# Kernel optimization log

Measured on AMD Instinct MI355X. Metric: run time of the kernel, lower is better.

Reference implementation:

```python
import jax, jax.numpy as jnp
import numpy as np
import math

B, S, D, H = 2, 2048, 1024, 16


def setup_inputs() -> dict:
    key = jax.random.key(0)
    ks = jax.random.split(key, 5)
    sc = 0.02  # small init scale for weights
    return {
        "x": jax.random.normal(ks[0], (B, S, D), dtype=jnp.float32),
        "Wqkv_w": jax.random.normal(ks[1], (3 * D, D), dtype=jnp.float32) * sc,
        "Wqkv_b": jnp.zeros((3 * D,), jnp.float32),
        "sel_w": jax.random.normal(ks[2], (1, D), dtype=jnp.float32) * sc,
        "sel_b": jnp.zeros((1,), jnp.float32),
        "out_w": jax.random.normal(ks[3], (D, D), dtype=jnp.float32) * sc,
        "out_b": jnp.zeros((D,), jnp.float32),
    }


def reference(x, Wqkv_w, Wqkv_b, sel_w, sel_b, out_w, out_b):
    b, s, d = x.shape
    h = H
    hd = d // h
    # Wqkv projection -> (b, s, 3, h, hd)
    qkv = (x @ Wqkv_w.T + Wqkv_b).reshape(b, s, 3, h, hd)
    q, k, v = qkv[:, :, 0], qkv[:, :, 1], qkv[:, :, 2]
    scale = 1.0 / math.sqrt(hd)
    scores = jnp.einsum('bthd,bshd->bhts', q, k * scale)  # (b,h,s,s)
    causal_mask = jnp.triu(jnp.full((s, s), -10000.0, dtype=scores.dtype), 1)
    attn = jax.nn.softmax(scores + causal_mask, axis=-1)
    ctx = jnp.einsum('bhts,bshd->bthd', attn, v).reshape(b, s, d)
    attn_out = ctx @ out_w.T + out_b  # (b,s,d)
    # selection: softmax over sequence dim, scaled by sqrt(d)/8
    sel = jax.nn.softmax(x @ sel_w.T + sel_b, axis=1) * (math.sqrt(d) / 8.0)  # (b,s,1)
    # eval path: topk over sequence, gather, scatter_add into x
    kk = math.ceil(math.sqrt(s))  # 46 for s=2048
    _, idx = jax.lax.top_k(sel[..., 0], kk)  # (b,kk) indices into seq dim
    val = attn_out * sel  # (b,s,d)
    bidx = jnp.arange(b)[:, None]
    src = val[bidx, idx]  # gather -> (b,kk,d)
    y = x.at[bidx, idx].add(src)  # scatter_add
    return y
```

## Files before the change

### kernel.cpp

```cpp
#include <hip/hip_runtime.h>
#include <stdint.h>

#define BATCH 2
#define SEQ   2048
#define DIM   1024
#define NH    16
#define HD    64
#define KK    46
#define NSEL  (BATCH*KK)
#define MPAD  128
#define CHUNK 128
#define NCH   (SEQ/CHUNK)
#define QP    48
#define SPLITK 8

typedef __attribute__((ext_vector_type(8))) short short8;
typedef __attribute__((ext_vector_type(4))) float f32x4;

__device__ inline unsigned short f2bf(float f) {
  union { float f; uint32_t u; } v; v.f = f;
  uint32_t u = v.u;
  uint32_t r = u + 0x7fff + ((u >> 16) & 1);
  return (unsigned short)(r >> 16);
}
__device__ inline float bf2f(unsigned short h) {
  union { uint32_t u; float f; } v; v.u = ((uint32_t)h) << 16;
  return v.f;
}
__device__ inline uint32_t f2ord(float f) {
  union { float f; uint32_t u; } v; v.f = f;
  return (v.u & 0x80000000u) ? ~v.u : (v.u | 0x80000000u);
}

__device__ inline void gload16(const void* g, void* l) {
  __builtin_amdgcn_global_load_lds(
      (const __attribute__((address_space(1))) void*)g,
      (__attribute__((address_space(3))) void*)l, 16, 0, 0);
}

__global__ __launch_bounds__(256) void prep_kernel(
    const float* __restrict__ wqkv, const float* __restrict__ outw,
    unsigned short* __restrict__ wqkvb, unsigned short* __restrict__ outwb,
    const float* __restrict__ x, unsigned short* __restrict__ xb,
    const float* __restrict__ sel_w, const float* __restrict__ sel_b,
    float* __restrict__ z, float* __restrict__ out)
{
  if (blockIdx.x < 2048) {
    int i = (blockIdx.x * 256 + threadIdx.x) * 8;
    const int NW = 3 * DIM * DIM;
    const float* src; unsigned short* dst; int j;
    if (i < NW) { src = wqkv; dst = wqkvb; j = i; }
    else        { src = outw; dst = outwb; j = i - NW; }
    float4 a = *(const float4*)(src + j);
    float4 b = *(const float4*)(src + j + 4);
    ushort4 o0, o1;
    o0.x = f2bf(a.x); o0.y = f2bf(a.y); o0.z = f2bf(a.z); o0.w = f2bf(a.w);
    o1.x = f2bf(b.x); o1.y = f2bf(b.y); o1.z = f2bf(b.z); o1.w = f2bf(b.w);
    *(ushort4*)(dst + j)     = o0;
    *(ushort4*)(dst + j + 4) = o1;
  } else {
    int wave = threadIdx.x >> 6, lane = threadIdx.x & 63;
    int row = (blockIdx.x - 2048) * 4 + wave;
    const float* xr = x + (size_t)row * DIM;
    unsigned short* xo = xb + (size_t)row * DIM;
    float* oo = out + (size_t)row * DIM;
    float s = 0.f;
#pragma unroll
    for (int it = 0; it < 4; ++it) {
      int c = it * 256 + lane * 4;
      float4 xv = *(const float4*)(xr + c);
      float4 wv = *(const float4*)(sel_w + c);
      s += xv.x*wv.x + xv.y*wv.y + xv.z*wv.z + xv.w*wv.w;
      ushort4 o;
      o.x = f2bf(xv.x); o.y = f2bf(xv.y); o.z = f2bf(xv.z); o.w = f2bf(xv.w);
      *(ushort4*)(xo + c) = o;
      *(float4*)(oo + c) = xv;
    }
#pragma unroll
    for (int o = 32; o > 0; o >>= 1) s += __shfl_xor(s, o);
    if (lane == 0) z[row] = s + sel_b[0];
  }
}

__global__ __launch_bounds__(256) void topk_kernel(const float* __restrict__ z,
                                                   float* __restrict__ sel,
                                                   int* __restrict__ idxout)
{
  int b = blockIdx.x, t = threadIdx.x;
  int lane = t & 63, wid = t >> 6;
  __shared__ int   hist[256];
  __shared__ float fred[4];
  __shared__ int   ired[4];
  __shared__ int   s_B, s_need;
  __shared__ float s_mx, s_sum;

  int s0 = t * 8;
  float zz[8];
  uint32_t uu[8];
  {
    float4 a = *(const float4*)(z + b*SEQ + s0);
    float4 c = *(const float4*)(z + b*SEQ + s0 + 4);
    zz[0]=a.x; zz[1]=a.y; zz[2]=a.z; zz[3]=a.w;
    zz[4]=c.x; zz[5]=c.y; zz[6]=c.z; zz[7]=c.w;
  }
#pragma unroll
  for (int i = 0; i < 8; ++i) uu[i] = f2ord(zz[i]);

  float lm = zz[0];
#pragma unroll
  for (int i = 1; i < 8; ++i) lm = fmaxf(lm, zz[i]);
#pragma unroll
  for (int o = 32; o > 0; o >>= 1) lm = fmaxf(lm, __shfl_xor(lm, o));
  if (lane == 0) fred[wid] = lm;
  __syncthreads();
  if (t == 0) s_mx = fmaxf(fmaxf(fred[0], fred[1]), fmaxf(fred[2], fred[3]));
  __syncthreads();
  float mx = s_mx;

  float pp[8];
  float ls = 0.f;
#pragma unroll
  for (int i = 0; i < 8; ++i) { pp[i] = __expf(zz[i] - mx); ls += pp[i]; }
#pragma unroll
  for (int o = 32; o > 0; o >>= 1) ls += __shfl_xor(ls, o);
  if (lane == 0) fred[wid] = ls;
  __syncthreads();
  if (t == 0) s_sum = fred[0] + fred[1] + fred[2] + fred[3];
  __syncthreads();
  float sscale = 4.0f / s_sum;
#pragma unroll
  for (int i = 0; i < 8; ++i) sel[b*SEQ + s0 + i] = pp[i] * sscale;

  uint32_t pref = 0;
  int need = KK;
#pragma unroll
  for (int pass = 0; pass < 4; ++pass) {
    int shift = 24 - pass * 8;
    uint32_t maskhi = pass ? (0xFFFFFFFFu << (shift + 8)) : 0u;
    hist[t] = 0;
    __syncthreads();
#pragma unroll
    for (int i = 0; i < 8; ++i) {
      if ((uu[i] & maskhi) == pref)
        atomicAdd(&hist[(uu[i] >> shift) & 255], 1);
    }
    __syncthreads();
    if (t < 64) {
      int c0 = hist[t*4], c1 = hist[t*4+1], c2 = hist[t*4+2], c3 = hist[t*4+3];
      int sl = c0 + c1 + c2 + c3;
      int suf = sl;
#pragma unroll
      for (int off = 1; off < 64; off <<= 1) {
        int o = __shfl_down(suf, off);
        if (lane + off < 64) suf += o;
      }
      int above = suf - sl;
      if (above < need && above + sl >= need) {
        int cum = above;
        int cs[4] = {c0, c1, c2, c3};
#pragma unroll
        for (int k = 3; k >= 0; --k) {
          if (cum < need && cum + cs[k] >= need) {
            s_B = t*4 + k;
            s_need = need - cum;
            break;
          }
          cum += cs[k];
        }
      }
    }
    __syncthreads();
    pref |= ((uint32_t)s_B) << shift;
    need = s_need;
    __syncthreads();
  }
  uint32_t T = pref;

  int cgt = 0, ceq = 0;
#pragma unroll
  for (int i = 0; i < 8; ++i) { cgt += (uu[i] > T); ceq += (uu[i] == T); }
  int pack = (cgt << 12) | ceq;
  int inc = pack;
#pragma unroll
  for (int off = 1; off < 64; off <<= 1) {
    int o = __shfl_up(inc, off);
    if (lane >= off) inc += o;
  }
  if (lane == 63) ired[wid] = inc;
  __syncthreads();
  int wbase = 0;
  if (wid == 1) wbase = ired[0];
  else if (wid == 2) wbase = ired[0] + ired[1];
  else if (wid == 3) wbase = ired[0] + ired[1] + ired[2];
  int ex = wbase + inc - pack;
  int g = ex >> 12, e = ex & 0xFFF;
#pragma unroll
  for (int i = 0; i < 8; ++i) {
    int s = s0 + i;
    bool isgt = uu[i] > T;
    bool iseq = uu[i] == T;
    int rank = -1;
    if (isgt) rank = g + (e < need ? e : need);
    else if (iseq && e < need) rank = g + e;
    if (rank >= 0) idxout[b*KK + rank] = s;
    g += isgt; e += iseq;
  }
}

__global__ __launch_bounds__(256) void gemms_kernel(
    const unsigned short* __restrict__ xb,
    const unsigned short* __restrict__ wqkvb,
    const float* __restrict__ Wqkv_b,
    unsigned short* __restrict__ kvb,
    float* __restrict__ qpart,
    const int* __restrict__ idxp)
{
  __shared__ unsigned short As[2][128*32];
  __shared__ unsigned short Bs[2][128*32];
  int tid  = threadIdx.x;
  int lane = tid & 63, wave = tid >> 6;
  int wr = (wave >> 1) * 64, wc = (wave & 1) * 64;
  int lr = lane & 15;
  int sx = (((lane >> 4) ^ ((lane >> 1) & 3)) << 3);
  int srow = lane >> 2;
  int scol = (((lane & 3) ^ ((lane >> 3) & 3)) << 3);
  int rb = 4 * (lane >> 4);

  if (blockIdx.x < 512) {
    const unsigned short* Bw = wqkvb + (size_t)DIM * DIM;
    int flat = blockIdx.x;
    int xcd = flat & 7, i8 = flat >> 3;
    int tile = xcd * 64 + i8;
    int bx = tile & 15, by = tile >> 4;
    int bm = by * 128, bn = bx * 128;
    const int K = DIM, N = 2 * DIM;

    const unsigned short* ap[2];
    const unsigned short* bp[2];
#pragma unroll
    for (int c = 0; c < 2; ++c) {
      int row = (wave * 2 + c) * 16 + srow;
      ap[c] = xb + (size_t)(bm + row) * K + scol;
      bp[c] = Bw + (size_t)(bn + row) * K + scol;
    }
    f32x4 acc[4][4] = {};
#pragma unroll
    for (int c = 0; c < 2; ++c) {
      int ch = wave * 2 + c;
      gload16(ap[c], (char*)As[0] + ch * 1024 + lane * 16);
      gload16(bp[c], (char*)Bs[0] + ch * 1024 + lane * 16);
      ap[c] += 32; bp[c] += 32;
    }
    __syncthreads();
    int cur = 0;
    for (int t = 0; t < 32; ++t) {
      if (t + 1 < 32) {
#pragma unroll
        for (int c = 0; c < 2; ++c) {
          int ch = wave * 2 + c;
          gload16(ap[c], (char*)As[cur ^ 1] + ch * 1024 + lane * 16);
          gload16(bp[c], (char*)Bs[cur ^ 1] + ch * 1024 + lane * 16);
          ap[c] += 32; bp[c] += 32;
        }
      }
      short8 af[4], bf[4];
#pragma unroll
      for (int m = 0; m < 4; ++m) af[m] = *(const short8*)&As[cur][(wr + m*16 + lr)*32 + sx];
#pragma unroll
      for (int n = 0; n < 4; ++n) bf[n] = *(const short8*)&Bs[cur][(wc + n*16 + lr)*32 + sx];
#pragma unroll
      for (int m = 0; m < 4; ++m)
#pragma unroll
        for (int n = 0; n < 4; ++n)
          acc[m][n] = __builtin_amdgcn_mfma_f32_16x16x32_bf16(af[m], bf[n], acc[m][n], 0, 0, 0);
      __syncthreads();
      cur ^= 1;
    }
#pragma unroll
    for (int m = 0; m < 4; ++m) {
#pragma unroll
      for (int n = 0; n < 4; ++n) {
        int col = bn + wc + n*16 + lr;
        float bv = Wqkv_b[DIM + col];
#pragma unroll
        for (int i = 0; i < 4; ++i) {
          int row = bm + wr + m*16 + rb + i;
          kvb[(size_t)row * N + col] = f2bf(acc[m][n][i] + bv);
        }
      }
    }
  } else {
    int bi = blockIdx.x - 512;
    int sk = bi >> 3;
    int bn = (bi & 7) * 128;
    int kb = sk * 128;
    const int K = DIM, N = DIM;

    const unsigned short* ap[2];
    const unsigned short* bp[2];
#pragma unroll
    for (int c = 0; c < 2; ++c) {
      int row = (wave * 2 + c) * 16 + srow;
      int bb = 0, rr = 0;
      if (row < NSEL) { bb = row / KK; rr = idxp[row]; }
      ap[c] = xb + ((size_t)(bb * SEQ + rr)) * K + kb + scol;
      bp[c] = wqkvb + (size_t)(bn + row) * K + kb + scol;
    }
    f32x4 acc[4][4] = {};
#pragma unroll
    for (int c = 0; c < 2; ++c) {
      int ch = wave * 2 + c;
      gload16(ap[c], (char*)As[0] + ch * 1024 + lane * 16);
      gload16(bp[c], (char*)Bs[0] + ch * 1024 + lane * 16);
      ap[c] += 32; bp[c] += 32;
    }
    __syncthreads();
    int cur = 0;
    for (int t = 0; t < 4; ++t) {
      if (t + 1 < 4) {
#pragma unroll
        for (int c = 0; c < 2; ++c) {
          int ch = wave * 2 + c;
          gload16(ap[c], (char*)As[cur ^ 1] + ch * 1024 + lane * 16);
          gload16(bp[c], (char*)Bs[cur ^ 1] + ch * 1024 + lane * 16);
          ap[c] += 32; bp[c] += 32;
        }
      }
      short8 af[4], bf[4];
#pragma unroll
      for (int m = 0; m < 4; ++m) af[m] = *(const short8*)&As[cur][(wr + m*16 + lr)*32 + sx];
#pragma unroll
      for (int n = 0; n < 4; ++n) bf[n] = *(const short8*)&Bs[cur][(wc + n*16 + lr)*32 + sx];
#pragma unroll
      for (int m = 0; m < 4; ++m)
#pragma unroll
        for (int n = 0; n < 4; ++n)
          acc[m][n] = __builtin_amdgcn_mfma_f32_16x16x32_bf16(af[m], bf[n], acc[m][n], 0, 0, 0);
      __syncthreads();
      cur ^= 1;
    }
    float* po = qpart + (size_t)sk * MPAD * N;
#pragma unroll
    for (int m = 0; m < 4; ++m) {
#pragma unroll
      for (int n = 0; n < 4; ++n) {
        int col = bn + wc + n*16 + lr;
#pragma unroll
        for (int i = 0; i < 4; ++i) {
          int row = wr + m*16 + rb + i;
          po[(size_t)row * N + col] = acc[m][n][i];
        }
      }
    }
  }
}

__global__ __launch_bounds__(256) void gemm_splitk_kernel(
    const unsigned short* __restrict__ A,
    const unsigned short* __restrict__ Bw,
    float* __restrict__ part, int N, int K)
{
  __shared__ unsigned short As[2][128*32];
  __shared__ unsigned short Bs[2][128*32];
  int tid  = threadIdx.x;
  int lane = tid & 63, wave = tid >> 6;
  int wr = (wave >> 1) * 64, wc = (wave & 1) * 64;
  int bn = blockIdx.x * 128;
  int sk = blockIdx.z;
  int ksl = K / SPLITK;
  int kb  = sk * ksl;

  int lr = lane & 15;
  int sx = (((lane >> 4) ^ ((lane >> 1) & 3)) << 3);
  int srow = lane >> 2;
  int scol = (((lane & 3) ^ ((lane >> 3) & 3)) << 3);

  const unsigned short* ap[2];
  const unsigned short* bp[2];
#pragma unroll
  for (int c = 0; c < 2; ++c) {
    int row = (wave * 2 + c) * 16 + srow;
    ap[c] = A  + (size_t)row * K + kb + scol;
    bp[c] = Bw + (size_t)(bn + row) * K + kb + scol;
  }

  f32x4 acc[4][4] = {};
  int nt = ksl / 32;
#pragma unroll
  for (int c = 0; c < 2; ++c) {
    int ch = wave * 2 + c;
    gload16(ap[c], (char*)As[0] + ch * 1024 + lane * 16);
    gload16(bp[c], (char*)Bs[0] + ch * 1024 + lane * 16);
    ap[c] += 32; bp[c] += 32;
  }
  __syncthreads();

  int cur = 0;
  for (int t = 0; t < nt; ++t) {
    if (t + 1 < nt) {
#pragma unroll
      for (int c = 0; c < 2; ++c) {
        int ch = wave * 2 + c;
        gload16(ap[c], (char*)As[cur ^ 1] + ch * 1024 + lane * 16);
        gload16(bp[c], (char*)Bs[cur ^ 1] + ch * 1024 + lane * 16);
        ap[c] += 32; bp[c] += 32;
      }
    }
    short8 af[4], bf[4];
#pragma unroll
    for (int m = 0; m < 4; ++m) af[m] = *(const short8*)&As[cur][(wr + m*16 + lr)*32 + sx];
#pragma unroll
    for (int n = 0; n < 4; ++n) bf[n] = *(const short8*)&Bs[cur][(wc + n*16 + lr)*32 + sx];
#pragma unroll
    for (int m = 0; m < 4; ++m)
#pragma unroll
      for (int n = 0; n < 4; ++n)
        acc[m][n] = __builtin_amdgcn_mfma_f32_16x16x32_bf16(af[m], bf[n], acc[m][n], 0, 0, 0);
    __syncthreads();
    cur ^= 1;
  }

  int rb = 4 * (lane >> 4);
  float* po = part + (size_t)sk * MPAD * N;
#pragma unroll
  for (int m = 0; m < 4; ++m) {
#pragma unroll
    for (int n = 0; n < 4; ++n) {
      int col = bn + wc + n*16 + lr;
#pragma unroll
      for (int i = 0; i < 4; ++i) {
        int row = wr + m*16 + rb + i;
        po[(size_t)row * N + col] = acc[m][n][i];
      }
    }
  }
}

__global__ void qcombine_kernel(const float* __restrict__ part,
                                const float* __restrict__ bias,
                                unsigned short* __restrict__ qgb)
{
  int i = (blockIdx.x * 256 + threadIdx.x) * 4;
  int col = i & (DIM - 1);
  float4 a = *(const float4*)(bias + col);
#pragma unroll
  for (int sk = 0; sk < SPLITK; ++sk) {
    float4 p = *(const float4*)(part + (size_t)sk * MPAD * DIM + i);
    a.x += p.x; a.y += p.y; a.z += p.z; a.w += p.w;
  }
  ushort4 o;
  o.x = f2bf(a.x); o.y = f2bf(a.y); o.z = f2bf(a.z); o.w = f2bf(a.w);
  *(ushort4*)(qgb + i) = o;
}

__global__ __launch_bounds__(256) void attn_chunk_kernel(
    const unsigned short* __restrict__ qgb,
    const unsigned short* __restrict__ kvb,
    const int* __restrict__ idx,
    float* __restrict__ Opart,
    float* __restrict__ mpart,
    float* __restrict__ lpart)
{
  int h = blockIdx.x, b = blockIdx.y, kc = blockIdx.z;
  int t = threadIdx.x, lane = t & 63, w = t >> 6;
  int lr = lane & 15, hk = lane >> 4;

  __shared__ unsigned short Qs[QP][72];
  __shared__ union { unsigned short Ks[CHUNK][72]; unsigned short ps[QP][136]; } U;
  __shared__ unsigned short Vt[HD][134];
  __shared__ int   rsi[QP];
  __shared__ float wred[4][QP];
  __shared__ float wsum[4][QP];

  if (t < QP) rsi[t] = (t < KK) ? idx[b*KK + t] : -1;
  for (int i = t; i < QP*8; i += 256) {
    int q = i >> 3, c8 = (i & 7) * 8;
    uint4 v;
    if (q < KK) v = *(const uint4*)(qgb + (size_t)(b*KK + q)*DIM + h*HD + c8);
    else        { v.x = 0; v.y = 0; v.z = 0; v.w = 0; }
    *(uint4*)&Qs[q][c8] = v;
  }
  for (int i = t; i < CHUNK*8; i += 256) {
    int r = i >> 3, c8 = (i & 7) * 8;
    *(uint4*)&U.Ks[r][c8] =
      *(const uint4*)(kvb + ((size_t)(b*SEQ + kc*CHUNK + r))*2048 + h*HD + c8);
  }
  for (int i = t; i < CHUNK*8; i += 256) {
    int r = i >> 3, d8 = (i & 7) * 8;
    uint4 v = *(const uint4*)(kvb + ((size_t)(b*SEQ + kc*CHUNK + r))*2048 + DIM + h*HD + d8);
    const unsigned short* pv = (const unsigned short*)&v;
#pragma unroll
    for (int j = 0; j < 8; ++j) Vt[d8 + j][r] = pv[j];
  }
  __syncthreads();

  short8 af[3][2], bfr[2][2];
#pragma unroll
  for (int m = 0; m < 3; ++m)
#pragma unroll
    for (int kk = 0; kk < 2; ++kk)
      af[m][kk] = *(const short8*)&Qs[m*16 + lr][kk*32 + hk*8];
#pragma unroll
  for (int j = 0; j < 2; ++j)
#pragma unroll
    for (int kk = 0; kk < 2; ++kk)
      bfr[j][kk] = *(const short8*)&U.Ks[(2*w + j)*16 + lr][kk*32 + hk*8];
  f32x4 acc[3][2] = {};
#pragma unroll
  for (int kk = 0; kk < 2; ++kk)
#pragma unroll
    for (int m = 0; m < 3; ++m)
#pragma unroll
      for (int j = 0; j < 2; ++j)
        acc[m][j] = __builtin_amdgcn_mfma_f32_16x16x32_bf16(af[m][kk], bfr[j][kk], acc[m][j], 0, 0, 0);

  float s[3][2][4];
  float rmax[3][4];
#pragma unroll
  for (int m = 0; m < 3; ++m)
#pragma unroll
    for (int reg = 0; reg < 4; ++reg) {
      int row = m*16 + hk*4 + reg;
      int rq = rsi[row];
      float mx = -3e38f;
#pragma unroll
      for (int j = 0; j < 2; ++j) {
        int gkey = kc*CHUNK + (2*w + j)*16 + lr;
        float v = acc[m][j][reg] * 0.125f;
        if (gkey > rq) v = -3e38f;
        s[m][j][reg] = v;
        mx = fmaxf(mx, v);
      }
#pragma unroll
      for (int o = 1; o < 16; o <<= 1) mx = fmaxf(mx, __shfl_xor(mx, o));
      rmax[m][reg] = mx;
    }
  if (lr == 0) {
#pragma unroll
    for (int m = 0; m < 3; ++m)
#pragma unroll
      for (int reg = 0; reg < 4; ++reg)
        wred[w][m*16 + hk*4 + reg] = rmax[m][reg];
  }
  __syncthreads();

  float rsum[3][4];
#pragma unroll
  for (int m = 0; m < 3; ++m)
#pragma unroll
    for (int reg = 0; reg < 4; ++reg) {
      int row = m*16 + hk*4 + reg;
      float gm = fmaxf(fmaxf(wred[0][row], wred[1][row]), fmaxf(wred[2][row], wred[3][row]));
      gm = fmaxf(gm, -1e37f);
      float sum = 0.f;
#pragma unroll
      for (int j = 0; j < 2; ++j) {
        float p = __expf(s[m][j][reg] - gm);
        sum += p;
        U.ps[row][(2*w + j)*16 + lr] = f2bf(p);
      }
#pragma unroll
      for (int o = 1; o < 16; o <<= 1) sum += __shfl_xor(sum, o);
      rsum[m][reg] = sum;
      rmax[m][reg] = gm;
    }
  if (lr == 0) {
#pragma unroll
    for (int m = 0; m < 3; ++m)
#pragma unroll
      for (int reg = 0; reg < 4; ++reg)
        wsum[w][m*16 + hk*4 + reg] = rsum[m][reg];
  }
  __syncthreads();

  if (w == 0 && lr == 0) {
    size_t base = ((size_t)(b*NH + h)*NCH + kc)*KK;
#pragma unroll
    for (int m = 0; m < 3; ++m)
#pragma unroll
      for (int reg = 0; reg < 4; ++reg) {
        int row = m*16 + hk*4 + reg;
        if (row < KK) {
          float L = wsum[0][row] + wsum[1][row] + wsum[2][row] + wsum[3][row];
          mpart[base + row] = rmax[m][reg];
          lpart[base + row] = L;
        }
      }
  }

  f32x4 acc2[3] = {};
#pragma unroll
  for (int kt = 0; kt < 4; ++kt) {
    short8 bv = *(const short8*)&Vt[w*16 + lr][kt*32 + hk*8];
#pragma unroll
    for (int m = 0; m < 3; ++m) {
      short8 av = *(const short8*)&U.ps[m*16 + lr][kt*32 + hk*8];
      acc2[m] = __builtin_amdgcn_mfma_f32_16x16x32_bf16(av, bv, acc2[m], 0, 0, 0);
    }
  }
  size_t obase = (((size_t)(b*NH + h)*NCH + kc)*KK)*HD;
#pragma unroll
  for (int m = 0; m < 3; ++m)
#pragma unroll
    for (int reg = 0; reg < 4; ++reg) {
      int q = m*16 + hk*4 + reg;
      if (q < KK) Opart[obase + (size_t)q*HD + w*16 + lr] = acc2[m][reg];
    }
}

__global__ __launch_bounds__(64) void attn_combine_kernel(
    const float* __restrict__ Opart,
    const float* __restrict__ mpart,
    const float* __restrict__ lpart,
    unsigned short* __restrict__ ctxg)
{
  int h = blockIdx.x, j = blockIdx.y;
  int b = j / KK, q = j % KK;
  int d = threadIdx.x;
  size_t mb = (size_t)(b*NH + h)*NCH;
  float M = -3e38f;
#pragma unroll
  for (int c = 0; c < NCH; ++c) M = fmaxf(M, mpart[(mb + c)*KK + q]);
  float L = 0.f, o = 0.f;
#pragma unroll
  for (int c = 0; c < NCH; ++c) {
    float f = __expf(mpart[(mb + c)*KK + q] - M);
    L += lpart[(mb + c)*KK + q] * f;
    o = fmaf(Opart[((mb + c)*KK + q)*HD + d], f, o);
  }
  ctxg[(size_t)j*DIM + h*HD + d] = f2bf(o / L);
}

__global__ void rowfix_kernel(const float* __restrict__ x,
                              const float* __restrict__ apart,
                              const float* __restrict__ out_b,
                              const float* __restrict__ sel,
                              const int* __restrict__ idx,
                              float* __restrict__ out)
{
  int j = blockIdx.x;
  int b = j / KK;
  int r = idx[j];
  int col = threadIdx.x * 4;
  size_t off = ((size_t)(b * SEQ + r)) * DIM + col;
  float s = sel[b * SEQ + r];
  float4 a = *(const float4*)(out_b + col);
#pragma unroll
  for (int sk = 0; sk < SPLITK; ++sk) {
    float4 p = *(const float4*)(apart + ((size_t)sk * MPAD + j) * DIM + col);
    a.x += p.x; a.y += p.y; a.z += p.z; a.w += p.w;
  }
  float4 v = *(const float4*)(x + off);
  v.x += a.x * s; v.y += a.y * s; v.z += a.z * s; v.w += a.w * s;
  *(float4*)(out + off) = v;
}

extern "C" void kernel_launch(void* const* d_in, const int* in_sizes, int n_in,
                              void* d_out, int out_size, void* d_ws, size_t ws_size,
                              hipStream_t stream)
{
  (void)in_sizes; (void)n_in; (void)out_size; (void)ws_size;
  const float* x      = (const float*)d_in[0];
  const float* Wqkv_w = (const float*)d_in[1];
  const float* Wqkv_b = (const float*)d_in[2];
  const float* sel_w  = (const float*)d_in[3];
  const float* sel_b  = (const float*)d_in[4];
  const float* out_w  = (const float*)d_in[5];
  const float* out_b  = (const float*)d_in[6];
  float* out = (float*)d_out;
  char* ws = (char*)d_ws;

  unsigned short* xb    = (unsigned short*)(ws);
  unsigned short* wqkvb = (unsigned short*)(ws + (8u  << 20));
  unsigned short* outwb = (unsigned short*)(ws + (14u << 20));
  unsigned short* kvb   = (unsigned short*)(ws + (16u << 20));
  float* z      = (float*)(ws + (32u << 20));
  float* sel    = (float*)(ws + (32u << 20) + (16u << 10));
  int*   idx    = (int*)  (ws + (32u << 20) + (32u << 10));
  unsigned short* ctxg = (unsigned short*)(ws + (33u << 20) + (256u << 10));
  unsigned short* qgb  = (unsigned short*)(ws + (33u << 20) + (512u << 10));
  float* Opart = (float*)(ws + (35u << 20));
  float* mpart = (float*)(ws + (42u << 20));
  float* lpart = (float*)(ws + (42u << 20) + (256u << 10));
  float* qpart = (float*)(ws + (44u << 20));
  float* apart = (float*)(ws + (48u << 20));

  prep_kernel<<<3072, 256, 0, stream>>>(Wqkv_w, out_w, wqkvb, outwb,
                                        x, xb, sel_w, sel_b, z, out);
  topk_kernel<<<BATCH, 256, 0, stream>>>(z, sel, idx);

  gemms_kernel<<<576, 256, 0, stream>>>(xb, wqkvb, Wqkv_b, kvb, qpart, idx);
  qcombine_kernel<<<MPAD*DIM/1024, 256, 0, stream>>>(qpart, Wqkv_b, qgb);

  dim3 gac(NH, BATCH, NCH);
  attn_chunk_kernel<<<gac, 256, 0, stream>>>(qgb, kvb, idx, Opart, mpart, lpart);
  dim3 gcb(NH, NSEL);
  attn_combine_kernel<<<gcb, 64, 0, stream>>>(Opart, mpart, lpart, ctxg);

  dim3 gsk(DIM/128, 1, SPLITK);
  gemm_splitk_kernel<<<gsk, 256, 0, stream>>>(ctxg, outwb, apart, DIM, DIM);

  rowfix_kernel<<<NSEL, 256, 0, stream>>>(x, apart, out_b, sel, idx, out);
}
```

Baseline: 76.14 us.

## Use single-wave 64x64 GEMM tiles, drop Q split-K and its combine kernel

Both GEMM kernels now run one 64-lane wave per block on 64x64 tiles, with barrier-free double buffering that waits on vmcnt. The K/V projection becomes 2048 smaller tiles. The selected-row Q projection runs the full K loop per tile and writes bf16 output with bias directly, which removes the qpart buffer and the qcombine launch. The out-projection uses 64x64 tiles over two M blocks, so it only covers the 92 real rows plus a little padding. The trade-off is less data reuse per block and lower per-block MFMA occupancy, while the Q path loses its split-K parallelism.

```diff
diff --git a/kernel.cpp b/kernel.cpp
--- a/kernel.cpp
+++ b/kernel.cpp
@@ -207,250 +207,194 @@
   }
 }
 
-__global__ __launch_bounds__(256) void gemms_kernel(
+__global__ __launch_bounds__(64) void gemms_kernel(
     const unsigned short* __restrict__ xb,
     const unsigned short* __restrict__ wqkvb,
     const float* __restrict__ Wqkv_b,
     unsigned short* __restrict__ kvb,
-    float* __restrict__ qpart,
+    unsigned short* __restrict__ qgb,
     const int* __restrict__ idxp)
 {
-  __shared__ unsigned short As[2][128*32];
-  __shared__ unsigned short Bs[2][128*32];
-  int tid  = threadIdx.x;
-  int lane = tid & 63, wave = tid >> 6;
-  int wr = (wave >> 1) * 64, wc = (wave & 1) * 64;
+  __shared__ unsigned short As[2][64*32];
+  __shared__ unsigned short Bs[2][64*32];
+  int lane = threadIdx.x;
   int lr = lane & 15;
   int sx = (((lane >> 4) ^ ((lane >> 1) & 3)) << 3);
-  int srow = lane >> 2;
+  int crow = lane >> 2;
   int scol = (((lane & 3) ^ ((lane >> 3) & 3)) << 3);
   int rb = 4 * (lane >> 4);
 
-  if (blockIdx.x < 512) {
+  const unsigned short* ap[4];
+  const unsigned short* bp[4];
+  int bm, bn, nt;
+  bool isKV = blockIdx.x < 2048;
+  const int K = DIM;
+
+  if (isKV) {
+    int flat = blockIdx.x;
+    int tile = (flat & 7) * 256 + (flat >> 3);
+    int bx = tile & 31, by = tile >> 5;
+    bm = by * 64; bn = bx * 64;
+    nt = 32;
     const unsigned short* Bw = wqkvb + (size_t)DIM * DIM;
-    int flat = blockIdx.x;
-    int xcd = flat & 7, i8 = flat >> 3;
-    int tile = xcd * 64 + i8;
-    int bx = tile & 15, by = tile >> 4;
-    int bm = by * 128, bn = bx * 128;
-    const int K = DIM, N = 2 * DIM;
-
-    const unsigned short* ap[2];
-    const unsigned short* bp[2];
-#pragma unroll
-    for (int c = 0; c < 2; ++c) {
-      int row = (wave * 2 + c) * 16 + srow;
+#pragma unroll
+    for (int c = 0; c < 4; ++c) {
+      int row = c * 16 + crow;
       ap[c] = xb + (size_t)(bm + row) * K + scol;
       bp[c] = Bw + (size_t)(bn + row) * K + scol;
     }
-    f32x4 acc[4][4] = {};
-#pragma unroll
-    for (int c = 0; c < 2; ++c) {
-      int ch = wave * 2 + c;
-      gload16(ap[c], (char*)As[0] + ch * 1024 + lane * 16);
-      gload16(bp[c], (char*)Bs[0] + ch * 1024 + lane * 16);
-      ap[c] += 32; bp[c] += 32;
-    }
-    __syncthreads();
-    int cur = 0;
-    for (int t = 0; t < 32; ++t) {
-      if (t + 1 < 32) {
-#pragma unroll
-        for (int c = 0; c < 2; ++c) {
-          int ch = wave * 2 + c;
-          gload16(ap[c], (char*)As[cur ^ 1] + ch * 1024 + lane * 16);
-          gload16(bp[c], (char*)Bs[cur ^ 1] + ch * 1024 + lane * 16);
-          ap[c] += 32; bp[c] += 32;
-        }
-      }
-      short8 af[4], bf[4];
-#pragma unroll
-      for (int m = 0; m < 4; ++m) af[m] = *(const short8*)&As[cur][(wr + m*16 + lr)*32 + sx];
-#pragma unroll
-      for (int n = 0; n < 4; ++n) bf[n] = *(const short8*)&Bs[cur][(wc + n*16 + lr)*32 + sx];
-#pragma unroll
-      for (int m = 0; m < 4; ++m)
-#pragma unroll
-        for (int n = 0; n < 4; ++n)
-          acc[m][n] = __builtin_amdgcn_mfma_f32_16x16x32_bf16(af[m], bf[n], acc[m][n], 0, 0, 0);
-      __syncthreads();
-      cur ^= 1;
-    }
+  } else {
+    int bi = blockIdx.x - 2048;
+    bm = (bi >> 4) * 64;
+    bn = (bi & 15) * 64;
+    nt = 32;
+#pragma unroll
+    for (int c = 0; c < 4; ++c) {
+      int row = bm + c * 16 + crow;
+      int bb = 0, rr = 0;
+      if (row < NSEL) { bb = row / KK; rr = idxp[row]; }
+      ap[c] = xb + ((size_t)(bb * SEQ + rr)) * K + scol;
+      bp[c] = wqkvb + (size_t)(bn + c * 16 + crow) * K + scol;
+    }
+  }
+
+#pragma unroll
+  for (int c = 0; c < 4; ++c) {
+    gload16(ap[c], (char*)As[0] + c * 1024 + lane * 16);
+    gload16(bp[c], (char*)Bs[0] + c * 1024 + lane * 16);
+    ap[c] += 32; bp[c] += 32;
+  }
+
+  f32x4 acc[4][4] = {};
+  for (int t = 0; t < nt; ++t) {
+    asm volatile("s_waitcnt vmcnt(0)" ::: "memory");
+    __builtin_amdgcn_sched_barrier(0);
+    int cur = t & 1;
+    short8 af[4], bf[4];
+#pragma unroll
+    for (int m = 0; m < 4; ++m) af[m] = *(const short8*)&As[cur][(m*16 + lr)*32 + sx];
+#pragma unroll
+    for (int n = 0; n < 4; ++n) bf[n] = *(const short8*)&Bs[cur][(n*16 + lr)*32 + sx];
+    if (t + 1 < nt) {
+#pragma unroll
+      for (int c = 0; c < 4; ++c) {
+        gload16(ap[c], (char*)As[cur ^ 1] + c * 1024 + lane * 16);
+        gload16(bp[c], (char*)Bs[cur ^ 1] + c * 1024 + lane * 16);
+        ap[c] += 32; bp[c] += 32;
+      }
+    }
+#pragma unroll
+    for (int m = 0; m < 4; ++m)
+#pragma unroll
+      for (int n = 0; n < 4; ++n)
+        acc[m][n] = __builtin_amdgcn_mfma_f32_16x16x32_bf16(af[m], bf[n], acc[m][n], 0, 0, 0);
+  }
+
+  if (isKV) {
+    const int N = 2 * DIM;
 #pragma unroll
     for (int m = 0; m < 4; ++m) {
 #pragma unroll
       for (int n = 0; n < 4; ++n) {
-        int col = bn + wc + n*16 + lr;
+        int col = bn + n*16 + lr;
         float bv = Wqkv_b[DIM + col];
 #pragma unroll
         for (int i = 0; i < 4; ++i) {
-          int row = bm + wr + m*16 + rb + i;
+          int row = bm + m*16 + rb + i;
           kvb[(size_t)row * N + col] = f2bf(acc[m][n][i] + bv);
         }
       }
     }
   } else {
-    int bi = blockIdx.x - 512;
-    int sk = bi >> 3;
-    int bn = (bi & 7) * 128;
-    int kb = sk * 128;
-    const int K = DIM, N = DIM;
-
-    const unsigned short* ap[2];
-    const unsigned short* bp[2];
-#pragma unroll
-    for (int c = 0; c < 2; ++c) {
-      int row = (wave * 2 + c) * 16 + srow;
-      int bb = 0, rr = 0;
-      if (row < NSEL) { bb = row / KK; rr = idxp[row]; }
-      ap[c] = xb + ((size_t)(bb * SEQ + rr)) * K + kb + scol;
-      bp[c] = wqkvb + (size_t)(bn + row) * K + kb + scol;
-    }
-    f32x4 acc[4][4] = {};
-#pragma unroll
-    for (int c = 0; c < 2; ++c) {
-      int ch = wave * 2 + c;
-      gload16(ap[c], (char*)As[0] + ch * 1024 + lane * 16);
-      gload16(bp[c], (char*)Bs[0] + ch * 1024 + lane * 16);
-      ap[c] += 32; bp[c] += 32;
-    }
-    __syncthreads();
-    int cur = 0;
-    for (int t = 0; t < 4; ++t) {
-      if (t + 1 < 4) {
-#pragma unroll
-        for (int c = 0; c < 2; ++c) {
-          int ch = wave * 2 + c;
-          gload16(ap[c], (char*)As[cur ^ 1] + ch * 1024 + lane * 16);
-          gload16(bp[c], (char*)Bs[cur ^ 1] + ch * 1024 + lane * 16);
-          ap[c] += 32; bp[c] += 32;
+#pragma unroll
+    for (int m = 0; m < 4; ++m) {
+#pragma unroll
+      for (int n = 0; n < 4; ++n) {
+        int col = bn + n*16 + lr;
+        float bv = Wqkv_b[col];
+#pragma unroll
+        for (int i = 0; i < 4; ++i) {
+          int row = bm + m*16 + rb + i;
+          if (row < NSEL) qgb[(size_t)row * DIM + col] = f2bf(acc[m][n][i] + bv);
         }
       }
-      short8 af[4], bf[4];
-#pragma unroll
-      for (int m = 0; m < 4; ++m) af[m] = *(const short8*)&As[cur][(wr + m*16 + lr)*32 + sx];
-#pragma unroll
-      for (int n = 0; n < 4; ++n) bf[n] = *(const short8*)&Bs[cur][(wc + n*16 + lr)*32 + sx];
-#pragma unroll
-      for (int m = 0; m < 4; ++m)
-#pragma unroll
-        for (int n = 0; n < 4; ++n)
-          acc[m][n] = __builtin_amdgcn_mfma_f32_16x16x32_bf16(af[m], bf[n], acc[m][n], 0, 0, 0);
-      __syncthreads();
-      cur ^= 1;
-    }
-    float* po = qpart + (size_t)sk * MPAD * N;
-#pragma unroll
-    for (int m = 0; m < 4; ++m) {
-#pragma unroll
-      for (int n = 0; n < 4; ++n) {
-        int col = bn + wc + n*16 + lr;
-#pragma unroll
-        for (int i = 0; i < 4; ++i) {
-          int row = wr + m*16 + rb + i;
-          po[(size_t)row * N + col] = acc[m][n][i];
-        }
-      }
-    }
-  }
-}
-
-__global__ __launch_bounds__(256) void gemm_splitk_kernel(
+    }
+  }
+}
+
+__global__ __launch_bounds__(64) void outproj_kernel(
     const unsigned short* __restrict__ A,
     const unsigned short* __restrict__ Bw,
-    float* __restrict__ part, int N, int K)
-{
-  __shared__ unsigned short As[2][128*32];
-  __shared__ unsigned short Bs[2][128*32];
-  int tid  = threadIdx.x;
-  int lane = tid & 63, wave = tid >> 6;
-  int wr = (wave >> 1) * 64, wc = (wave & 1) * 64;
-  int bn = blockIdx.x * 128;
-  int sk = blockIdx.z;
-  int ksl = K / SPLITK;
-  int kb  = sk * ksl;
-
+    float* __restrict__ part)
+{
+  __shared__ unsigned short As[2][64*32];
+  __shared__ unsigned short Bs[2][64*32];
+  int lane = threadIdx.x;
   int lr = lane & 15;
   int sx = (((lane >> 4) ^ ((lane >> 1) & 3)) << 3);
-  int srow = lane >> 2;
+  int crow = lane >> 2;
   int scol = (((lane & 3) ^ ((lane >> 3) & 3)) << 3);
-
-  const unsigned short* ap[2];
-  const unsigned short* bp[2];
-#pragma unroll
-  for (int c = 0; c < 2; ++c) {
-    int row = (wave * 2 + c) * 16 + srow;
-    ap[c] = A  + (size_t)row * K + kb + scol;
+  int rb = 4 * (lane >> 4);
+
+  int bn = blockIdx.x * 64;
+  int bm = blockIdx.y * 64;
+  int sk = blockIdx.z;
+  int kb = sk * (DIM / SPLITK);
+  const int K = DIM, nt = (DIM / SPLITK) / 32;
+
+  const unsigned short* ap[4];
+  const unsigned short* bp[4];
+#pragma unroll
+  for (int c = 0; c < 4; ++c) {
+    int row = c * 16 + crow;
+    ap[c] = A  + (size_t)(bm + row) * K + kb + scol;
     bp[c] = Bw + (size_t)(bn + row) * K + kb + scol;
   }
+#pragma unroll
+  for (int c = 0; c < 4; ++c) {
+    gload16(ap[c], (char*)As[0] + c * 1024 + lane * 16);
+    gload16(bp[c], (char*)Bs[0] + c * 1024 + lane * 16);
+    ap[c] += 32; bp[c] += 32;
+  }
 
   f32x4 acc[4][4] = {};
-  int nt = ksl / 32;
-#pragma unroll
-  for (int c = 0; c < 2; ++c) {
-    int ch = wave * 2 + c;
-    gload16(ap[c], (char*)As[0] + ch * 1024 + lane * 16);
-    gload16(bp[c], (char*)Bs[0] + ch * 1024 + lane * 16);
-    ap[c] += 32; bp[c] += 32;
-  }
-  __syncthreads();
-
-  int cur = 0;
   for (int t = 0; t < nt; ++t) {
+    asm volatile("s_waitcnt vmcnt(0)" ::: "memory");
+    __builtin_amdgcn_sched_barrier(0);
+    int cur = t & 1;
+    short8 af[4], bf[4];
+#pragma unroll
+    for (int m = 0; m < 4; ++m) af[m] = *(const short8*)&As[cur][(m*16 + lr)*32 + sx];
+#pragma unroll
+    for (int n = 0; n < 4; ++n) bf[n] = *(const short8*)&Bs[cur][(n*16 + lr)*32 + sx];
     if (t + 1 < nt) {
 #pragma unroll
-      for (int c = 0; c < 2; ++c) {
-        int ch = wave * 2 + c;
-        gload16(ap[c], (char*)As[cur ^ 1] + ch * 1024 + lane * 16);
-        gload16(bp[c], (char*)Bs[cur ^ 1] + ch * 1024 + lane * 16);
+      for (int c = 0; c < 4; ++c) {
+        gload16(ap[c], (char*)As[cur ^ 1] + c * 1024 + lane * 16);
+        gload16(bp[c], (char*)Bs[cur ^ 1] + c * 1024 + lane * 16);
         ap[c] += 32; bp[c] += 32;
       }
     }
-    short8 af[4], bf[4];
-#pragma unroll
-    for (int m = 0; m < 4; ++m) af[m] = *(const short8*)&As[cur][(wr + m*16 + lr)*32 + sx];
-#pragma unroll
-    for (int n = 0; n < 4; ++n) bf[n] = *(const short8*)&Bs[cur][(wc + n*16 + lr)*32 + sx];
 #pragma unroll
     for (int m = 0; m < 4; ++m)
 #pragma unroll
       for (int n = 0; n < 4; ++n)
         acc[m][n] = __builtin_amdgcn_mfma_f32_16x16x32_bf16(af[m], bf[n], acc[m][n], 0, 0, 0);
-    __syncthreads();
-    cur ^= 1;
-  }
-
-  int rb = 4 * (lane >> 4);
-  float* po = part + (size_t)sk * MPAD * N;
+  }
+
+  float* po = part + (size_t)sk * MPAD * DIM;
 #pragma unroll
   for (int m = 0; m < 4; ++m) {
 #pragma unroll
     for (int n = 0; n < 4; ++n) {
-      int col = bn + wc + n*16 + lr;
+      int col = bn + n*16 + lr;
 #pragma unroll
       for (int i = 0; i < 4; ++i) {
-        int row = wr + m*16 + rb + i;
-        po[(size_t)row * N + col] = acc[m][n][i];
-      }
-    }
-  }
-}
-
-__global__ void qcombine_kernel(const float* __restrict__ part,
-                                const float* __restrict__ bias,
-                                unsigned short* __restrict__ qgb)
-{
-  int i = (blockIdx.x * 256 + threadIdx.x) * 4;
-  int col = i & (DIM - 1);
-  float4 a = *(const float4*)(bias + col);
-#pragma unroll
-  for (int sk = 0; sk < SPLITK; ++sk) {
-    float4 p = *(const float4*)(part + (size_t)sk * MPAD * DIM + i);
-    a.x += p.x; a.y += p.y; a.z += p.z; a.w += p.w;
-  }
-  ushort4 o;
-  o.x = f2bf(a.x); o.y = f2bf(a.y); o.z = f2bf(a.z); o.w = f2bf(a.w);
-  *(ushort4*)(qgb + i) = o;
+        int row = bm + m*16 + rb + i;
+        po[(size_t)row * DIM + col] = acc[m][n][i];
+      }
+    }
+  }
 }
 
 __global__ __launch_bounds__(256) void attn_chunk_kernel(
@@ -682,23 +626,21 @@
   float* Opart = (float*)(ws + (35u << 20));
   float* mpart = (float*)(ws + (42u << 20));
   float* lpart = (float*)(ws + (42u << 20) + (256u << 10));
-  float* qpart = (float*)(ws + (44u << 20));
   float* apart = (float*)(ws + (48u << 20));
 
   prep_kernel<<<3072, 256, 0, stream>>>(Wqkv_w, out_w, wqkvb, outwb,
                                         x, xb, sel_w, sel_b, z, out);
   topk_kernel<<<BATCH, 256, 0, stream>>>(z, sel, idx);
 
-  gemms_kernel<<<576, 256, 0, stream>>>(xb, wqkvb, Wqkv_b, kvb, qpart, idx);
-  qcombine_kernel<<<MPAD*DIM/1024, 256, 0, stream>>>(qpart, Wqkv_b, qgb);
+  gemms_kernel<<<2080, 64, 0, stream>>>(xb, wqkvb, Wqkv_b, kvb, qgb, idx);
 
   dim3 gac(NH, BATCH, NCH);
   attn_chunk_kernel<<<gac, 256, 0, stream>>>(qgb, kvb, idx, Opart, mpart, lpart);
   dim3 gcb(NH, NSEL);
   attn_combine_kernel<<<gcb, 64, 0, stream>>>(Opart, mpart, lpart, ctxg);
 
-  dim3 gsk(DIM/128, 1, SPLITK);
-  gemm_splitk_kernel<<<gsk, 256, 0, stream>>>(ctxg, outwb, apart, DIM, DIM);
+  dim3 gop(16, 2, SPLITK);
+  outproj_kernel<<<gop, 64, 0, stream>>>(ctxg, outwb, apart);
 
   rowfix_kernel<<<NSEL, 256, 0, stream>>>(x, apart, out_b, sel, idx, out);
 }
```

After: 83.52 us. +9.7%, slower.

## Triple-buffer GEMM LDS tiles with one barrier per K-step and vmcnt waits

Applied to the files above, without the earlier changes.

Moves the GEMM main loops from double-buffered to triple-buffered shared-memory staging. Two tiles are prefetched ahead, each step waits with explicit s_waitcnt vmcnt, and one raw s_barrier per iteration replaces the trailing __syncthreads. This aims to hide global-load latency better and halve barrier count, at the cost of 50% more LDS per block (48KB), which could reduce occupancy. The split-K kernel now hardcodes nt=4, assuming K/SPLITK==128.

```diff
diff --git a/kernel.cpp b/kernel.cpp
--- a/kernel.cpp
+++ b/kernel.cpp
@@ -215,8 +215,8 @@
     float* __restrict__ qpart,
     const int* __restrict__ idxp)
 {
-  __shared__ unsigned short As[2][128*32];
-  __shared__ unsigned short Bs[2][128*32];
+  __shared__ unsigned short As[3][128*32];
+  __shared__ unsigned short Bs[3][128*32];
   int tid  = threadIdx.x;
   int lane = tid & 63, wave = tid >> 6;
   int wr = (wave >> 1) * 64, wc = (wave & 1) * 64;
@@ -233,7 +233,7 @@
     int tile = xcd * 64 + i8;
     int bx = tile & 15, by = tile >> 4;
     int bm = by * 128, bn = bx * 128;
-    const int K = DIM, N = 2 * DIM;
+    const int K = DIM, N = 2 * DIM, nt = 32;
 
     const unsigned short* ap[2];
     const unsigned short* bp[2];
@@ -245,36 +245,43 @@
     }
     f32x4 acc[4][4] = {};
 #pragma unroll
-    for (int c = 0; c < 2; ++c) {
-      int ch = wave * 2 + c;
-      gload16(ap[c], (char*)As[0] + ch * 1024 + lane * 16);
-      gload16(bp[c], (char*)Bs[0] + ch * 1024 + lane * 16);
-      ap[c] += 32; bp[c] += 32;
-    }
-    __syncthreads();
+    for (int pb = 0; pb < 2; ++pb) {
+#pragma unroll
+      for (int c = 0; c < 2; ++c) {
+        int ch = wave * 2 + c;
+        gload16(ap[c], (char*)As[pb] + ch * 1024 + lane * 16);
+        gload16(bp[c], (char*)Bs[pb] + ch * 1024 + lane * 16);
+        ap[c] += 32; bp[c] += 32;
+      }
+    }
     int cur = 0;
-    for (int t = 0; t < 32; ++t) {
-      if (t + 1 < 32) {
+    for (int t = 0; t < nt; ++t) {
+      if (t + 1 < nt) asm volatile("s_waitcnt vmcnt(4)" ::: "memory");
+      else            asm volatile("s_waitcnt vmcnt(0)" ::: "memory");
+      __builtin_amdgcn_s_barrier();
+      asm volatile("" ::: "memory");
+      __builtin_amdgcn_sched_barrier(0);
+      short8 af[4], bf[4];
+#pragma unroll
+      for (int m = 0; m < 4; ++m) af[m] = *(const short8*)&As[cur][(wr + m*16 + lr)*32 + sx];
+#pragma unroll
+      for (int n = 0; n < 4; ++n) bf[n] = *(const short8*)&Bs[cur][(wc + n*16 + lr)*32 + sx];
+      if (t + 2 < nt) {
+        int nb = cur + 2; if (nb >= 3) nb -= 3;
 #pragma unroll
         for (int c = 0; c < 2; ++c) {
           int ch = wave * 2 + c;
-          gload16(ap[c], (char*)As[cur ^ 1] + ch * 1024 + lane * 16);
-          gload16(bp[c], (char*)Bs[cur ^ 1] + ch * 1024 + lane * 16);
+          gload16(ap[c], (char*)As[nb] + ch * 1024 + lane * 16);
+          gload16(bp[c], (char*)Bs[nb] + ch * 1024 + lane * 16);
           ap[c] += 32; bp[c] += 32;
         }
       }
-      short8 af[4], bf[4];
-#pragma unroll
-      for (int m = 0; m < 4; ++m) af[m] = *(const short8*)&As[cur][(wr + m*16 + lr)*32 + sx];
-#pragma unroll
-      for (int n = 0; n < 4; ++n) bf[n] = *(const short8*)&Bs[cur][(wc + n*16 + lr)*32 + sx];
 #pragma unroll
       for (int m = 0; m < 4; ++m)
 #pragma unroll
         for (int n = 0; n < 4; ++n)
           acc[m][n] = __builtin_amdgcn_mfma_f32_16x16x32_bf16(af[m], bf[n], acc[m][n], 0, 0, 0);
-      __syncthreads();
-      cur ^= 1;
+      cur = (cur + 1 == 3) ? 0 : cur + 1;
     }
 #pragma unroll
     for (int m = 0; m < 4; ++m) {
@@ -294,7 +301,7 @@
     int sk = bi >> 3;
     int bn = (bi & 7) * 128;
     int kb = sk * 128;
-    const int K = DIM, N = DIM;
+    const int K = DIM, N = DIM, nt = 4;
 
     const unsigned short* ap[2];
     const unsigned short* bp[2];
@@ -308,36 +315,43 @@
     }
     f32x4 acc[4][4] = {};
 #pragma unroll
-    for (int c = 0; c < 2; ++c) {
-      int ch = wave * 2 + c;
-      gload16(ap[c], (char*)As[0] + ch * 1024 + lane * 16);
-      gload16(bp[c], (char*)Bs[0] + ch * 1024 + lane * 16);
-      ap[c] += 32; bp[c] += 32;
-    }
-    __syncthreads();
+    for (int pb = 0; pb < 2; ++pb) {
+#pragma unroll
+      for (int c = 0; c < 2; ++c) {
+        int ch = wave * 2 + c;
+        gload16(ap[c], (char*)As[pb] + ch * 1024 + lane * 16);
+        gload16(bp[c], (char*)Bs[pb] + ch * 1024 + lane * 16);
+        ap[c] += 32; bp[c] += 32;
+      }
+    }
     int cur = 0;
-    for (int t = 0; t < 4; ++t) {
-      if (t + 1 < 4) {
+    for (int t = 0; t < nt; ++t) {
+      if (t + 1 < nt) asm volatile("s_waitcnt vmcnt(4)" ::: "memory");
+      else            asm volatile("s_waitcnt vmcnt(0)" ::: "memory");
+      __builtin_amdgcn_s_barrier();
+      asm volatile("" ::: "memory");
+      __builtin_amdgcn_sched_barrier(0);
+      short8 af[4], bf[4];
+#pragma unroll
+      for (int m = 0; m < 4; ++m) af[m] = *(const short8*)&As[cur][(wr + m*16 + lr)*32 + sx];
+#pragma unroll
+      for (int n = 0; n < 4; ++n) bf[n] = *(const short8*)&Bs[cur][(wc + n*16 + lr)*32 + sx];
+      if (t + 2 < nt) {
+        int nb = cur + 2; if (nb >= 3) nb -= 3;
 #pragma unroll
         for (int c = 0; c < 2; ++c) {
           int ch = wave * 2 + c;
-          gload16(ap[c], (char*)As[cur ^ 1] + ch * 1024 + lane * 16);
-          gload16(bp[c], (char*)Bs[cur ^ 1] + ch * 1024 + lane * 16);
+          gload16(ap[c], (char*)As[nb] + ch * 1024 + lane * 16);
+          gload16(bp[c], (char*)Bs[nb] + ch * 1024 + lane * 16);
           ap[c] += 32; bp[c] += 32;
         }
       }
-      short8 af[4], bf[4];
-#pragma unroll
-      for (int m = 0; m < 4; ++m) af[m] = *(const short8*)&As[cur][(wr + m*16 + lr)*32 + sx];
-#pragma unroll
-      for (int n = 0; n < 4; ++n) bf[n] = *(const short8*)&Bs[cur][(wc + n*16 + lr)*32 + sx];
 #pragma unroll
       for (int m = 0; m < 4; ++m)
 #pragma unroll
         for (int n = 0; n < 4; ++n)
           acc[m][n] = __builtin_amdgcn_mfma_f32_16x16x32_bf16(af[m], bf[n], acc[m][n], 0, 0, 0);
-      __syncthreads();
-      cur ^= 1;
+      cur = (cur + 1 == 3) ? 0 : cur + 1;
     }
     float* po = qpart + (size_t)sk * MPAD * N;
 #pragma unroll
@@ -360,8 +374,8 @@
     const unsigned short* __restrict__ Bw,
     float* __restrict__ part, int N, int K)
 {
-  __shared__ unsigned short As[2][128*32];
-  __shared__ unsigned short Bs[2][128*32];
+  __shared__ unsigned short As[3][128*32];
+  __shared__ unsigned short Bs[3][128*32];
   int tid  = threadIdx.x;
   int lane = tid & 63, wave = tid >> 6;
   int wr = (wave >> 1) * 64, wc = (wave & 1) * 64;
@@ -385,39 +399,45 @@
   }
 
   f32x4 acc[4][4] = {};
-  int nt = ksl / 32;
-#pragma unroll
-  for (int c = 0; c < 2; ++c) {
-    int ch = wave * 2 + c;
-    gload16(ap[c], (char*)As[0] + ch * 1024 + lane * 16);
-    gload16(bp[c], (char*)Bs[0] + ch * 1024 + lane * 16);
-    ap[c] += 32; bp[c] += 32;
-  }
-  __syncthreads();
-
+  const int nt = 4;
+#pragma unroll
+  for (int pb = 0; pb < 2; ++pb) {
+#pragma unroll
+    for (int c = 0; c < 2; ++c) {
+      int ch = wave * 2 + c;
+      gload16(ap[c], (char*)As[pb] + ch * 1024 + lane * 16);
+      gload16(bp[c], (char*)Bs[pb] + ch * 1024 + lane * 16);
+      ap[c] += 32; bp[c] += 32;
+    }
+  }
   int cur = 0;
   for (int t = 0; t < nt; ++t) {
-    if (t + 1 < nt) {
+    if (t + 1 < nt) asm volatile("s_waitcnt vmcnt(4)" ::: "memory");
+    else            asm volatile("s_waitcnt vmcnt(0)" ::: "memory");
+    __builtin_amdgcn_s_barrier();
+    asm volatile("" ::: "memory");
+    __builtin_amdgcn_sched_barrier(0);
+    short8 af[4], bf[4];
+#pragma unroll
+    for (int m = 0; m < 4; ++m) af[m] = *(const short8*)&As[cur][(wr + m*16 + lr)*32 + sx];
+#pragma unroll
+    for (int n = 0; n < 4; ++n) bf[n] = *(const short8*)&Bs[cur][(wc + n*16 + lr)*32 + sx];
+    if (t + 2 < nt) {
+      int nb = cur + 2; if (nb >= 3) nb -= 3;
 #pragma unroll
       for (int c = 0; c < 2; ++c) {
         int ch = wave * 2 + c;
-        gload16(ap[c], (char*)As[cur ^ 1] + ch * 1024 + lane * 16);
-        gload16(bp[c], (char*)Bs[cur ^ 1] + ch * 1024 + lane * 16);
+        gload16(ap[c], (char*)As[nb] + ch * 1024 + lane * 16);
+        gload16(bp[c], (char*)Bs[nb] + ch * 1024 + lane * 16);
         ap[c] += 32; bp[c] += 32;
       }
     }
-    short8 af[4], bf[4];
-#pragma unroll
-    for (int m = 0; m < 4; ++m) af[m] = *(const short8*)&As[cur][(wr + m*16 + lr)*32 + sx];
-#pragma unroll
-    for (int n = 0; n < 4; ++n) bf[n] = *(const short8*)&Bs[cur][(wc + n*16 + lr)*32 + sx];
 #pragma unroll
     for (int m = 0; m < 4; ++m)
 #pragma unroll
       for (int n = 0; n < 4; ++n)
         acc[m][n] = __builtin_amdgcn_mfma_f32_16x16x32_bf16(af[m], bf[n], acc[m][n], 0, 0, 0);
-    __syncthreads();
-    cur ^= 1;
+    cur = (cur + 1 == 3) ? 0 : cur + 1;
   }
 
   int rb = 4 * (lane >> 4);
```

Result: faster. 71.54 us (-6.0%).
